# Kernel optimization log

Measured on AMD Instinct MI355X. Metric: run time of the kernel, lower is better.

The kernel has to match this reference:

```python
import jax, jax.numpy as jnp
import numpy as np

N = 8192          # num_people
H = 128           # hidden_dim
ZE = 64           # zone_embed_dim
TE = 32           # temporal_embed_dim
NZ = 100          # num_zones
GRU_IN = H + ZE + TE


def _lin(k, out_d, in_d):
    kw, kb = jax.random.split(k)
    bound = 1.0 / np.sqrt(in_d)
    W = jax.random.uniform(kw, (out_d, in_d), minval=-bound, maxval=bound, dtype=jnp.float32)
    b = jax.random.uniform(kb, (out_d,), minval=-bound, maxval=bound, dtype=jnp.float32)
    return W, b


def setup_inputs() -> dict:
    key = jax.random.key(0)
    ks = jax.random.split(key, 12)
    t = jax.random.uniform(ks[0], (1,), dtype=jnp.float32)
    person_h = jax.random.normal(ks[1], (N, H), dtype=jnp.float32)
    gnn_zone_embeds = jax.random.normal(ks[2], (NZ, ZE), dtype=jnp.float32)
    W_time, b_time = _lin(ks[3], TE, 1)
    W_loc, b_loc = _lin(ks[4], NZ, H)
    Wq, bq = _lin(ks[5], H, H)
    Wk, bk = _lin(ks[6], H, H)
    Wv, bv = _lin(ks[7], H, H)
    W_merge, b_merge = _lin(ks[8], H, 2 * H)
    W_ih, b_ih = _lin(ks[9], 3 * H, GRU_IN)
    W_hh, b_hh = _lin(ks[10], 3 * H, H)
    ln_gamma = jnp.ones((H,), jnp.float32)
    ln_beta = jnp.zeros((H,), jnp.float32)
    return dict(t=t, person_h=person_h, gnn_zone_embeds=gnn_zone_embeds,
                W_time=W_time, b_time=b_time, W_loc=W_loc, b_loc=b_loc,
                Wq=Wq, bq=bq, Wk=Wk, bk=bk, Wv=Wv, bv=bv,
                W_merge=W_merge, b_merge=b_merge,
                W_ih=W_ih, b_ih=b_ih, W_hh=W_hh, b_hh=b_hh,
                ln_gamma=ln_gamma, ln_beta=ln_beta)


def reference(t, person_h, gnn_zone_embeds, W_time, b_time, W_loc, b_loc,
              Wq, bq, Wk, bk, Wv, bv, W_merge, b_merge,
              W_ih, b_ih, W_hh, b_hh, ln_gamma, ln_beta):
    n = person_h.shape[0]
    # spatial context: soft location distribution over zones
    loc_probs = jax.nn.softmax(person_h @ W_loc.T + b_loc, axis=-1)   # [N, NZ]
    spatial_context = loc_probs @ gnn_zone_embeds                     # [N, ZE]
    # leave-one-out social attention == full attention with diagonal masked
    q = person_h @ Wq.T + bq                                          # [N, H]
    k = person_h @ Wk.T + bk
    v = person_h @ Wv.T + bv
    scores = (q @ k.T) / np.sqrt(H).astype(np.float32)                # [N, N]
    diag = jnp.eye(n, dtype=bool)
    scores = jnp.where(diag, -jnp.inf, scores)
    attn = jax.nn.softmax(scores, axis=-1)
    social_context = attn @ v                                         # [N, H]
    h_interacted = jnp.concatenate([person_h, social_context], axis=-1) @ W_merge.T + b_merge
    time_context = jnp.broadcast_to(t.reshape(1, 1), (n, 1)) @ W_time.T + b_time  # [N, TE]
    gru_input = jnp.concatenate([h_interacted, spatial_context, time_context], axis=-1)
    # torch.nn.GRUCell: gates order (reset, update, new)
    gx = gru_input @ W_ih.T + b_ih                                    # [N, 3H]
    gh = person_h @ W_hh.T + b_hh
    xr, xz, xn = jnp.split(gx, 3, axis=-1)
    hr, hz, hn = jnp.split(gh, 3, axis=-1)
    r = jax.nn.sigmoid(xr + hr)
    z = jax.nn.sigmoid(xz + hz)
    ng = jnp.tanh(xn + r * hn)
    h_new = (1.0 - z) * ng + z * person_h
    d = h_new - person_h
    mu = jnp.mean(d, axis=-1, keepdims=True)
    var = jnp.var(d, axis=-1, keepdims=True)
    d = (d - mu) * jax.lax.rsqrt(var + 1e-5) * ln_gamma + ln_beta
    return d
```

## Files before the change

### kernel.cpp

```cpp
#include <hip/hip_runtime.h>


typedef __attribute__((ext_vector_type(8)))  short bf16x8;
typedef __attribute__((ext_vector_type(4)))  float f32x4;
typedef __attribute__((ext_vector_type(16))) float f32x16;
typedef __attribute__((ext_vector_type(4)))  unsigned uint4v;

#define N_P   8192
#define H_D   128
#define NCHNK 8
#define CHLEN (N_P / NCHNK)
#define KVB   64
#define NTIL  (CHLEN / KVB)
#define LDE   384

#if __has_builtin(__builtin_amdgcn_exp2f)
#define EXP2(x) __builtin_amdgcn_exp2f(x)
#else
#define EXP2(x) exp2f(x)
#endif

__device__ __forceinline__ short f2bf(float f) {
  unsigned u = __float_as_uint(f);
  u = (u + 0x7fffu + ((u >> 16) & 1u)) >> 16;
  return (short)u;
}
__device__ __forceinline__ float bf2f(short s) {
  return __uint_as_float(((unsigned)(unsigned short)s) << 16);
}

__device__ __forceinline__ int swzb(int row, int slot, int nslots) {
  return (row * nslots + (slot ^ (row & ((nslots - 1) & 7)))) << 4;
}

__device__ __forceinline__ unsigned cvtpk(float a, float b) {
  unsigned d;
  asm("v_cvt_pk_bf16_f32 %0, %1, %2" : "=v"(d) : "v"(a), "v"(b));
  return d;
}

__device__ __forceinline__ void swap32(unsigned& a, unsigned& b) {
#if __has_builtin(__builtin_amdgcn_permlane32_swap)
  auto r = __builtin_amdgcn_permlane32_swap(a, b, false, false);
  a = r[0]; b = r[1];
#else
  asm volatile("v_permlane32_swap_b32 %0, %1" : "+v"(a), "+v"(b));
#endif
}

typedef __attribute__((address_space(1))) const void GV;
typedef __attribute__((address_space(3))) void LV;
__device__ __forceinline__ void gld_lds16(const void* g, void* l) {
  __builtin_amdgcn_global_load_lds((GV*)g, (LV*)l, 16, 0, 0);
}

__constant__ const float QSCALE = 0.12751551485988857f;
#define LOG2E 1.4426950408889634f

__global__ __launch_bounds__(256) void init_kernel(
    const float* t, const float* W_time, const float* b_time,
    const float* W_loc, const float* b_loc,
    const float* Wq, const float* bq, const float* Wk, const float* bk,
    const float* Wv, const float* bv,
    const float* W_merge, const float* b_merge,
    const float* W_ih, const float* b_ih,
    const float* W_hh, const float* b_hh,
    const float* ph,
    short* W1, float* bias1, short* W_all, float* bias_gx, short* PH2e) {
  const int b = blockIdx.x, tidl = threadIdx.x;
  if (b < 64) {
    int tid = b * 256 + tidl, stride = 64 * 256;
    for (int i = tid; i < 896 * 128; i += stride) {
      int r = i >> 7, k = i & 127;
      float v;
      if (r < 128)      v = Wq[r * 128 + k];
      else if (r < 256) v = Wk[(r - 128) * 128 + k];
      else if (r < 384) v = Wv[(r - 256) * 128 + k];
      else if (r < 484) v = W_loc[(r - 384) * 128 + k];
      else if (r < 868) v = W_hh[(r - 484) * 128 + k];
      else              v = 0.f;
      W1[i] = f2bf(v);
    }
    for (int i = tid; i < 896; i += stride) {
      float v;
      if (i < 128)      v = bq[i];
      else if (i < 256) v = bk[i - 128];
      else if (i < 384) v = bv[i - 256];
      else if (i < 484) v = b_loc[i - 384];
      else if (i < 868) v = b_hh[i - 484];
      else              v = 0.f;
      bias1[i] = v;
    }
  } else if (b < 448) {
    __shared__ float rowj[128];
    const int n = b - 64;
    if (tidl < 128) rowj[tidl] = W_ih[n * 224 + tidl];
    __syncthreads();
    {
      float acc = 0.f;
#pragma unroll 8
      for (int j = 0; j < 128; ++j) acc += rowj[j] * W_merge[j * 256 + tidl];
      W_all[n * 384 + tidl] = f2bf(acc);
    }
    if (tidl < 128) {
      int k2 = 256 + tidl;
      float v;
      if (k2 < 320)      v = W_ih[n * 224 + 128 + (k2 - 256)];
      else if (k2 < 352) v = W_ih[n * 224 + 192 + (k2 - 320)];
      else               v = 0.f;
      W_all[n * 384 + k2] = f2bf(v);
    }
    if (tidl < 64) {
      float p = rowj[tidl] * b_merge[tidl] + rowj[tidl + 64] * b_merge[tidl + 64];
#pragma unroll
      for (int mk = 1; mk < 64; mk <<= 1) p += __shfl_xor(p, mk);
      if (tidl == 0) bias_gx[n] = b_ih[n] + p;
    }
  } else {
    int tid = (b - 448) * 256 + tidl, stride = 1024 * 256;
    for (int i = tid; i < N_P * H_D; i += stride) {
      int r = i >> 7, d = i & 127;
      PH2e[r * LDE + d] = f2bf(ph[i]);
    }
    const float t0 = t[0];
    for (int i = tid; i < N_P * 64; i += stride) {
      int r = i >> 6, j = i & 63;
      float v = (j < 32) ? (t0 * W_time[j] + b_time[j]) : 0.f;
      PH2e[r * LDE + 320 + j] = f2bf(v);
    }
  }
}

template <int MODE, int K>
__global__ __launch_bounds__(256, 3) void gemm64_kernel(
    const short* __restrict__ X, int ldx, const short* __restrict__ W,
    const float* __restrict__ bias,
    short* out_q, short* out_k, short* out_v, float* out_loc, short* out_gh,
    short* out_gx) {
  __shared__ short Xl[64 * 128];
  __shared__ short Wl[128 * 128];
  const int tid = threadIdx.x;
  const int bm = blockIdx.x * 64, bn = blockIdx.y * 128;
  const int l = tid & 63, wid = tid >> 6;
  const int g = l >> 4, c = l & 15;
  const int wr = wid >> 1, wc = wid & 1;
  f32x4 acc[2][4] = {};
  constexpr int KT = K / 128;
#pragma unroll 1
  for (int kt = 0; kt < KT; ++kt) {
    const int k0 = kt * 128;
#pragma unroll
    for (int pass = 0; pass < 4; ++pass) {
      int s = tid + pass * 256;
      int row = s >> 4, p = s & 15;
      int lsl = p ^ (row & 7);
      gld_lds16(X + (size_t)(bm + row) * ldx + k0 + lsl * 8, (char*)Xl + s * 16);
    }
#pragma unroll
    for (int pass = 0; pass < 8; ++pass) {
      int s = tid + pass * 256;
      int row = s >> 4, p = s & 15;
      int lsl = p ^ (row & 7);
      gld_lds16(W + (size_t)(bn + row) * K + k0 + lsl * 8, (char*)Wl + s * 16);
    }
    __syncthreads();
#pragma unroll
    for (int kc = 0; kc < 4; ++kc) {
      bf16x8 a[2], bfr[4];
#pragma unroll
      for (int mi = 0; mi < 2; ++mi)
        a[mi] = *(const bf16x8*)((const char*)Xl + swzb(wr * 32 + mi * 16 + c, kc * 4 + g, 16));
#pragma unroll
      for (int ni = 0; ni < 4; ++ni)
        bfr[ni] = *(const bf16x8*)((const char*)Wl + swzb(wc * 64 + ni * 16 + c, kc * 4 + g, 16));
#pragma unroll
      for (int mi = 0; mi < 2; ++mi)
#pragma unroll
        for (int ni = 0; ni < 4; ++ni)
          acc[mi][ni] = __builtin_amdgcn_mfma_f32_16x16x32_bf16(a[mi], bfr[ni], acc[mi][ni], 0, 0, 0);
    }
    if (kt + 1 < KT) __syncthreads();
  }
#pragma unroll
  for (int mi = 0; mi < 2; ++mi)
#pragma unroll
    for (int ni = 0; ni < 4; ++ni)
#pragma unroll
      for (int r = 0; r < 4; ++r) {
        int row = bm + wr * 32 + mi * 16 + 4 * g + r;
        int col = bn + wc * 64 + ni * 16 + c;
        float val = acc[mi][ni][r] + bias[col];
        if constexpr (MODE == 0) {
          if (col < 128)      out_q[row * 128 + col] = f2bf(val * QSCALE);
          else if (col < 256) out_k[row * 128 + col - 128] = f2bf(val);
          else if (col < 384) out_v[row * 128 + col - 256] = f2bf(val);
          else if (col < 484) out_loc[row * 112 + col - 384] = val;
          else if (col < 868) out_gh[row * 384 + col - 484] = f2bf(val);
        } else {
          out_gx[row * 384 + col] = f2bf(val);
        }
      }
}

__global__ __launch_bounds__(256) void tv_spatial_kernel(const short* __restrict__ vf,
                                                         short* __restrict__ vT,
                                                         const float* __restrict__ locf,
                                                         const float* __restrict__ E,
                                                         short* __restrict__ PH2e) {
  const int b = blockIdx.x, tid = threadIdx.x;
  if (b < 1024) {
    __shared__ short T[32][40];
    int tx = tid & 31, ty = tid >> 5;
    int bi = b >> 2, bd = b & 3;
#pragma unroll
    for (int k = 0; k < 4; ++k)
      T[ty + 8 * k][tx] = vf[(bi * 32 + ty + 8 * k) * 128 + bd * 32 + tx];
    __syncthreads();
#pragma unroll
    for (int k = 0; k < 4; ++k)
      vT[(size_t)(bd * 32 + ty + 8 * k) * N_P + bi * 32 + tx] = T[tx][ty + 8 * k];
  } else {
    __shared__ float pl[4][104];
    int wid = tid >> 6, l = tid & 63;
    int row = (b - 1024) * 4 + wid;
    float v0 = locf[row * 112 + l];
    float v1 = (l + 64 < 100) ? locf[row * 112 + 64 + l] : -1e30f;
    float m = fmaxf(v0, v1);
#pragma unroll
    for (int mk = 1; mk < 64; mk <<= 1) m = fmaxf(m, __shfl_xor(m, mk));
    float p0 = EXP2((v0 - m) * LOG2E);
    float p1 = (l + 64 < 100) ? EXP2((v1 - m) * LOG2E) : 0.f;
    float s = p0 + p1;
#pragma unroll
    for (int mk = 1; mk < 64; mk <<= 1) s += __shfl_xor(s, mk);
    float inv = 1.f / s;
    pl[wid][l] = p0 * inv;
    if (l + 64 < 100) pl[wid][64 + l] = p1 * inv;
    float acc = 0.f;
#pragma unroll 4
    for (int z = 0; z < 100; ++z) acc += pl[wid][z] * E[z * 64 + l];
    PH2e[row * LDE + 256 + l] = f2bf(acc);
  }
}

__global__ __launch_bounds__(256, 2) void attn_kernel(
    const short* __restrict__ qb, const short* __restrict__ kb,
    const short* __restrict__ vT, short* __restrict__ pacc,
    float* __restrict__ pml) {
  __shared__ short Kl[2][KVB * H_D];
  __shared__ short Vl[2][H_D * KVB];
  const int tid = threadIdx.x;
  const int qbk = blockIdx.x >> 3, ch = blockIdx.x & 7;
  const int chbase = ch * CHLEN;
  const int l = tid & 63, wid = tid >> 6;
  const int c32 = l & 31, hi = l >> 5;
  const int qrow0w = qbk * 128 + wid * 32;

  char* ldsK = (char*)&Kl[0][0];
  char* ldsV = (char*)&Vl[0][0];

  auto stage = [&](int b, int tt) {
    const int off = tt * KVB;
#pragma unroll
    for (int j = 0; j < 4; ++j) {
      const int i = tid + j * 256;
      const int kr = i >> 4, ks = (i & 15) ^ (kr & 15);
      gld_lds16(kb + (size_t)(chbase + off + kr) * 128 + ks * 8,
                ldsK + b * 16384 + i * 16);
      const int vr = i >> 3, vs = (i & 7) ^ (vr & 7);
      gld_lds16(vT + (size_t)vr * N_P + chbase + off + vs * 8,
                ldsV + b * 16384 + i * 16);
    }
  };

  bf16x8 qf[8];
#pragma unroll
  for (int sl = 0; sl < 8; ++sl)
    qf[sl] = *(const bf16x8*)(qb + (size_t)(qrow0w + c32) * 128 + sl * 16 + hi * 8);

  bf16x8 ones;
#pragma unroll
  for (int j = 0; j < 8; ++j) ones[j] = (short)0x3F80;

  const int c15 = c32 & 15;
  const int kbase0 = c32 * 256;
  int koff[8];
#pragma unroll
  for (int sl = 0; sl < 8; ++sl) koff[sl] = ((2 * sl + hi) ^ c15) << 4;
  const int xh = (c32 >> 1) & 3, x0 = c32 & 1;
  const int xb = (hi ^ x0) << 4;
  int voff[4], vbase[4];
#pragma unroll
  for (int s4 = 0; s4 < 4; ++s4) voff[s4] = (s4 ^ xh) << 5;
#pragma unroll
  for (int db = 0; db < 4; ++db) vbase[db] = (db * 32 + c32) * 128 + xb;

  f32x16 acc[4] = {};
  f32x16 accl = {};
  float m = -1e30f;

  stage(0, 0);
  asm volatile("s_waitcnt vmcnt(0)" ::: "memory");
  __builtin_amdgcn_s_barrier();
  int cur = 0;

#pragma unroll 1
  for (int t = 0; t < NTIL; ++t) {
    if (t + 1 < NTIL) stage(cur ^ 1, t + 1);

    const int kv0 = chbase + t * KVB;
    const char* Kb = (const char*)&Kl[cur][0];
    const char* Vb = (const char*)&Vl[cur][0];

    f32x16 s0 = {}, s1 = {};
    __builtin_amdgcn_s_setprio(1);
#pragma unroll
    for (int sl = 0; sl < 8; ++sl) {
      bf16x8 k0 = *(const bf16x8*)(Kb + kbase0 + koff[sl]);
      bf16x8 k1 = *(const bf16x8*)(Kb + kbase0 + 8192 + koff[sl]);
      s0 = __builtin_amdgcn_mfma_f32_32x32x16_bf16(k0, qf[sl], s0, 0, 0, 0);
      s1 = __builtin_amdgcn_mfma_f32_32x32x16_bf16(k1, qf[sl], s1, 0, 0, 0);
    }
    __builtin_amdgcn_s_setprio(0);

    if (qrow0w + 32 > kv0 && qrow0w < kv0 + 64) {
      const int qr = qrow0w + c32;
#pragma unroll
      for (int r = 0; r < 16; ++r) {
        const int rowp = (r & 3) + 8 * (r >> 2) + 4 * hi;
        s0[r] = (kv0 + rowp == qr) ? -1e30f : s0[r];
        s1[r] = (kv0 + 32 + rowp == qr) ? -1e30f : s1[r];
      }
    }

    if (t == 0) {
      f32x16 mx;
#pragma unroll
      for (int r = 0; r < 16; ++r) mx[r] = fmaxf(s0[r], s1[r]);
#pragma unroll
      for (int w2 = 8; w2 >= 1; w2 >>= 1)
#pragma unroll
        for (int r = 0; r < w2; ++r) mx[r] = fmaxf(mx[r], mx[r + w2]);
      m = fmaxf(mx[0], __shfl_xor(mx[0], 32));
    }

#pragma unroll
    for (int r = 0; r < 16; ++r) s0[r] = EXP2(s0[r] - m);
#pragma unroll
    for (int r = 0; r < 16; ++r) s1[r] = EXP2(s1[r] - m);

    auto pvslice = [&](const f32x16& ss, int base, int sl4) {
      unsigned dA = cvtpk(ss[base + 0], ss[base + 1]);
      unsigned dB = cvtpk(ss[base + 2], ss[base + 3]);
      unsigned dC = cvtpk(ss[base + 4], ss[base + 5]);
      unsigned dD = cvtpk(ss[base + 6], ss[base + 7]);
      swap32(dA, dC);
      swap32(dB, dD);
      uint4v w = {dA, dB, dC, dD};
      bf16x8 pa = __builtin_bit_cast(bf16x8, w);
#pragma unroll
      for (int db = 0; db < 4; ++db) {
        bf16x8 vfr = *(const bf16x8*)(Vb + vbase[db] + voff[sl4]);
        acc[db] = __builtin_amdgcn_mfma_f32_32x32x16_bf16(pa, vfr, acc[db], 0, 0, 0);
      }
      accl = __builtin_amdgcn_mfma_f32_32x32x16_bf16(pa, ones, accl, 0, 0, 0);
    };
    __builtin_amdgcn_s_setprio(1);
    pvslice(s0, 0, 0);
    pvslice(s0, 8, 1);
    pvslice(s1, 0, 2);
    pvslice(s1, 8, 3);
    __builtin_amdgcn_s_setprio(0);

    if (t + 1 < NTIL) {
      asm volatile("s_waitcnt vmcnt(0)" ::: "memory");
      __builtin_amdgcn_s_barrier();
      asm volatile("" ::: "memory");
    }
    cur ^= 1;
  }

#pragma unroll
  for (int db = 0; db < 4; ++db)
#pragma unroll
    for (int r = 0; r < 16; ++r) {
      const int qr = qrow0w + (r & 3) + 8 * (r >> 2) + 4 * hi;
      pacc[((size_t)ch * N_P + qr) * 128 + db * 32 + c32] = f2bf(acc[db][r]);
    }
  {
    const int rr = (c32 & 3) | (((c32 >> 3) & 3) << 2);
    float own = (((c32 >> 2) & 1) == hi) ? accl[rr] : 0.f;
    float lv = own + __shfl_xor(own, 32);
    if (hi == 0) {
      const int qr = qrow0w + c32;
      pml[((size_t)ch * N_P + qr) * 2]     = m;
      pml[((size_t)ch * N_P + qr) * 2 + 1] = lv;
    }
  }
}

__global__ __launch_bounds__(256) void combine_kernel(const short* __restrict__ pacc,
                                                      const float* __restrict__ pml,
                                                      short* __restrict__ PH2e) {
  int tid = threadIdx.x;
  int row = blockIdx.x * 2 + (tid >> 7);
  int d = tid & 127;
  float mv[NCHNK], lv[NCHNK], M = -1e30f;
#pragma unroll
  for (int cc = 0; cc < NCHNK; ++cc) {
    mv[cc] = pml[(cc * N_P + row) * 2];
    lv[cc] = pml[(cc * N_P + row) * 2 + 1];
    M = fmaxf(M, mv[cc]);
  }
  float L = 0.f, O = 0.f;
#pragma unroll
  for (int cc = 0; cc < NCHNK; ++cc) {
    float w = EXP2(mv[cc] - M);
    L += lv[cc] * w;
    O += bf2f(pacc[((size_t)cc * N_P + row) * 128 + d]) * w;
  }
  PH2e[row * LDE + 128 + d] = f2bf(O / L);
}

__global__ __launch_bounds__(256) void final_kernel(const short* __restrict__ gx,
                                                    const short* __restrict__ gh,
                                                    const float* __restrict__ ph,
                                                    const float* __restrict__ gamma,
                                                    const float* __restrict__ beta,
                                                    float* __restrict__ out) {
  int tid = threadIdx.x, wid = tid >> 6, l = tid & 63;
  int row = blockIdx.x * 4 + wid;
  float dd[2];
#pragma unroll
  for (int half = 0; half < 2; ++half) {
    int d = l + 64 * half;
    float h = ph[row * 128 + d];
    float xr = bf2f(gx[row * 384 + d]),       hr = bf2f(gh[row * 384 + d]);
    float xz = bf2f(gx[row * 384 + 128 + d]), hz = bf2f(gh[row * 384 + 128 + d]);
    float xn = bf2f(gx[row * 384 + 256 + d]), hn = bf2f(gh[row * 384 + 256 + d]);
    float r = 1.f / (1.f + EXP2(-LOG2E * (xr + hr)));
    float z = 1.f / (1.f + EXP2(-LOG2E * (xz + hz)));
    float a = xn + r * hn;
    float ng = 1.f - 2.f / (1.f + EXP2(2.f * LOG2E * a));
    dd[half] = (1.f - z) * (ng - h);
  }
  float s = dd[0] + dd[1], ss = dd[0] * dd[0] + dd[1] * dd[1];
#pragma unroll
  for (int mk = 1; mk < 64; mk <<= 1) {
    s += __shfl_xor(s, mk);
    ss += __shfl_xor(ss, mk);
  }
  float mu = s * (1.f / 128.f);
  float var = ss * (1.f / 128.f) - mu * mu;
  float rs = rsqrtf(var + 1e-5f);
#pragma unroll
  for (int half = 0; half < 2; ++half) {
    int d = l + 64 * half;
    out[row * 128 + d] = (dd[half] - mu) * rs * gamma[d] + beta[d];
  }
}

extern "C" void kernel_launch(void* const* d_in, const int* in_sizes, int n_in,
                              void* d_out, int out_size, void* d_ws, size_t ws_size,
                              hipStream_t stream) {
  const float* t       = (const float*)d_in[0];
  const float* ph      = (const float*)d_in[1];
  const float* E       = (const float*)d_in[2];
  const float* W_time  = (const float*)d_in[3];
  const float* b_time  = (const float*)d_in[4];
  const float* W_loc   = (const float*)d_in[5];
  const float* b_loc   = (const float*)d_in[6];
  const float* Wq      = (const float*)d_in[7];
  const float* bq      = (const float*)d_in[8];
  const float* Wk      = (const float*)d_in[9];
  const float* bk      = (const float*)d_in[10];
  const float* Wv      = (const float*)d_in[11];
  const float* bv      = (const float*)d_in[12];
  const float* W_merge = (const float*)d_in[13];
  const float* b_merge = (const float*)d_in[14];
  const float* W_ih    = (const float*)d_in[15];
  const float* b_ih    = (const float*)d_in[16];
  const float* W_hh    = (const float*)d_in[17];
  const float* b_hh    = (const float*)d_in[18];
  const float* gamma   = (const float*)d_in[19];
  const float* beta    = (const float*)d_in[20];
  float* out = (float*)d_out;

  char* w = (char*)d_ws;
  auto alloc = [&](size_t bytes) {
    char* p = w;
    w += (bytes + 255) & ~(size_t)255;
    return p;
  };
  short* W1     = (short*)alloc(896 * 128 * 2);
  float* bias1  = (float*)alloc(896 * 4);
  short* W_all  = (short*)alloc(384 * 384 * 2);
  float* bias_gx= (float*)alloc(384 * 4);
  short* PH2e   = (short*)alloc((size_t)N_P * LDE * 2);
  short* qbuf   = (short*)alloc((size_t)N_P * 128 * 2);
  short* kbuf   = (short*)alloc((size_t)N_P * 128 * 2);
  short* vf     = (short*)alloc((size_t)N_P * 128 * 2);
  short* vT     = (short*)alloc((size_t)128 * N_P * 2);
  float* locf   = (float*)alloc((size_t)N_P * 112 * 4);
  short* ghf    = (short*)alloc((size_t)N_P * 384 * 2);
  short* gx     = (short*)alloc((size_t)N_P * 384 * 2);
  short* pacc   = (short*)alloc((size_t)NCHNK * N_P * 128 * 2);
  float* pml    = (float*)alloc((size_t)NCHNK * N_P * 2 * 4);

  init_kernel<<<1472, 256, 0, stream>>>(t, W_time, b_time, W_loc, b_loc, Wq, bq,
                                        Wk, bk, Wv, bv, W_merge, b_merge,
                                        W_ih, b_ih, W_hh, b_hh, ph,
                                        W1, bias1, W_all, bias_gx, PH2e);
  gemm64_kernel<0, 128><<<dim3(128, 7), 256, 0, stream>>>(
      PH2e, LDE, W1, bias1, qbuf, kbuf, vf, locf, ghf, nullptr);
  tv_spatial_kernel<<<3072, 256, 0, stream>>>(vf, vT, locf, E, PH2e);
  attn_kernel<<<512, 256, 0, stream>>>(qbuf, kbuf, vT, pacc, pml);
  combine_kernel<<<4096, 256, 0, stream>>>(pacc, pml, PH2e);
  gemm64_kernel<2, 384><<<dim3(128, 3), 256, 0, stream>>>(
      PH2e, LDE, W_all, bias_gx, nullptr, nullptr, nullptr, nullptr, nullptr, gx);
  final_kernel<<<2048, 256, 0, stream>>>(gx, ghf, ph, gamma, beta, out);
}
```

Before: 97.32 us.

## Software-pipeline QK of next tile with softmax/PV and sum row totals on VALU

Restructures the attention loop so the QK^T MFMAs for the next KV tile run alongside the exp2 and PV work of the current tile. K and V staging are split, so K is prefetched two tiles ahead and V is issued after the barrier. The row-sum MFMA against a ones vector is replaced by a scalar fp32 accumulation of the exponentials. The aim is to hide softmax latency behind matrix work and to drop one MFMA per slice. The cost is higher register pressure from holding two score tiles at once, plus more intricate buffer reuse and synchronisation.

```diff
diff --git a/kernel.cpp b/kernel.cpp
--- a/kernel.cpp
+++ b/kernel.cpp
@@ -259,7 +259,7 @@
   char* ldsK = (char*)&Kl[0][0];
   char* ldsV = (char*)&Vl[0][0];
 
-  auto stage = [&](int b, int tt) {
+  auto stageK = [&](int b, int tt) {
     const int off = tt * KVB;
 #pragma unroll
     for (int j = 0; j < 4; ++j) {
@@ -267,6 +267,13 @@
       const int kr = i >> 4, ks = (i & 15) ^ (kr & 15);
       gld_lds16(kb + (size_t)(chbase + off + kr) * 128 + ks * 8,
                 ldsK + b * 16384 + i * 16);
+    }
+  };
+  auto stageV = [&](int b, int tt) {
+    const int off = tt * KVB;
+#pragma unroll
+    for (int j = 0; j < 4; ++j) {
+      const int i = tid + j * 256;
       const int vr = i >> 3, vs = (i & 7) ^ (vr & 7);
       gld_lds16(vT + (size_t)vr * N_P + chbase + off + vs * 8,
                 ldsV + b * 16384 + i * 16);
@@ -277,10 +284,6 @@
 #pragma unroll
   for (int sl = 0; sl < 8; ++sl)
     qf[sl] = *(const bf16x8*)(qb + (size_t)(qrow0w + c32) * 128 + sl * 16 + hi * 8);
-
-  bf16x8 ones;
-#pragma unroll
-  for (int j = 0; j < 8; ++j) ones[j] = (short)0x3F80;
 
   const int c15 = c32 & 15;
   const int kbase0 = c32 * 256;
@@ -296,59 +299,71 @@
   for (int db = 0; db < 4; ++db) vbase[db] = (db * 32 + c32) * 128 + xb;
 
   f32x16 acc[4] = {};
-  f32x16 accl = {};
-  float m = -1e30f;
-
-  stage(0, 0);
-  asm volatile("s_waitcnt vmcnt(0)" ::: "memory");
+  float m = -1e30f, lsum = 0.f;
+
+  auto qkTile = [&](const char* Kb, f32x16& o0, f32x16& o1, int sl) {
+    bf16x8 k0 = *(const bf16x8*)(Kb + kbase0 + koff[sl]);
+    bf16x8 k1 = *(const bf16x8*)(Kb + kbase0 + 8192 + koff[sl]);
+    o0 = __builtin_amdgcn_mfma_f32_32x32x16_bf16(k0, qf[sl], o0, 0, 0, 0);
+    o1 = __builtin_amdgcn_mfma_f32_32x32x16_bf16(k1, qf[sl], o1, 0, 0, 0);
+  };
+  auto maskTile = [&](f32x16& o0, f32x16& o1, int kv0) {
+    if (qrow0w + 32 > kv0 && qrow0w < kv0 + 64) {
+      const int qr = qrow0w + c32;
+#pragma unroll
+      for (int r = 0; r < 16; ++r) {
+        const int rowp = (r & 3) + 8 * (r >> 2) + 4 * hi;
+        o0[r] = (kv0 + rowp == qr) ? -1e30f : o0[r];
+        o1[r] = (kv0 + 32 + rowp == qr) ? -1e30f : o1[r];
+      }
+    }
+  };
+
+  stageK(0, 0); stageV(0, 0); stageK(1, 1); stageV(1, 1);
+  asm volatile("s_waitcnt vmcnt(4)" ::: "memory");
   __builtin_amdgcn_s_barrier();
-  int cur = 0;
+
+  f32x16 s0 = {}, s1 = {};
+#pragma unroll
+  for (int sl = 0; sl < 8; ++sl) qkTile(ldsK, s0, s1, sl);
+  maskTile(s0, s1, chbase);
+  {
+    f32x16 mx;
+#pragma unroll
+    for (int r = 0; r < 16; ++r) mx[r] = fmaxf(s0[r], s1[r]);
+#pragma unroll
+    for (int w2 = 8; w2 >= 1; w2 >>= 1)
+#pragma unroll
+      for (int r = 0; r < w2; ++r) mx[r] = fmaxf(mx[r], mx[r + w2]);
+    m = fmaxf(mx[0], __shfl_xor(mx[0], 32));
+  }
+  __builtin_amdgcn_s_barrier();
 
 #pragma unroll 1
   for (int t = 0; t < NTIL; ++t) {
-    if (t + 1 < NTIL) stage(cur ^ 1, t + 1);
-
-    const int kv0 = chbase + t * KVB;
-    const char* Kb = (const char*)&Kl[cur][0];
-    const char* Vb = (const char*)&Vl[cur][0];
-
-    f32x16 s0 = {}, s1 = {};
+    const int cur = t & 1, nxt = cur ^ 1;
+    if (t + 2 < NTIL) stageK(cur, t + 2);
+
     __builtin_amdgcn_s_setprio(1);
-#pragma unroll
-    for (int sl = 0; sl < 8; ++sl) {
-      bf16x8 k0 = *(const bf16x8*)(Kb + kbase0 + koff[sl]);
-      bf16x8 k1 = *(const bf16x8*)(Kb + kbase0 + 8192 + koff[sl]);
-      s0 = __builtin_amdgcn_mfma_f32_32x32x16_bf16(k0, qf[sl], s0, 0, 0, 0);
-      s1 = __builtin_amdgcn_mfma_f32_32x32x16_bf16(k1, qf[sl], s1, 0, 0, 0);
-    }
-    __builtin_amdgcn_s_setprio(0);
-
-    if (qrow0w + 32 > kv0 && qrow0w < kv0 + 64) {
-      const int qr = qrow0w + c32;
-#pragma unroll
-      for (int r = 0; r < 16; ++r) {
-        const int rowp = (r & 3) + 8 * (r >> 2) + 4 * hi;
-        s0[r] = (kv0 + rowp == qr) ? -1e30f : s0[r];
-        s1[r] = (kv0 + 32 + rowp == qr) ? -1e30f : s1[r];
+    f32x16 sn0 = {}, sn1 = {};
+    if (t + 1 < NTIL) {
+      const char* Kb = ldsK + nxt * 16384;
+#pragma unroll
+      for (int sl = 0; sl < 8; ++sl) {
+        qkTile(Kb, sn0, sn1, sl);
+        s0[2 * sl]     = EXP2(s0[2 * sl] - m);
+        s0[2 * sl + 1] = EXP2(s0[2 * sl + 1] - m);
+        s1[2 * sl]     = EXP2(s1[2 * sl] - m);
+        s1[2 * sl + 1] = EXP2(s1[2 * sl + 1] - m);
       }
-    }
-
-    if (t == 0) {
-      f32x16 mx;
-#pragma unroll
-      for (int r = 0; r < 16; ++r) mx[r] = fmaxf(s0[r], s1[r]);
-#pragma unroll
-      for (int w2 = 8; w2 >= 1; w2 >>= 1)
-#pragma unroll
-        for (int r = 0; r < w2; ++r) mx[r] = fmaxf(mx[r], mx[r + w2]);
-      m = fmaxf(mx[0], __shfl_xor(mx[0], 32));
-    }
-
-#pragma unroll
-    for (int r = 0; r < 16; ++r) s0[r] = EXP2(s0[r] - m);
-#pragma unroll
-    for (int r = 0; r < 16; ++r) s1[r] = EXP2(s1[r] - m);
-
+    } else {
+#pragma unroll
+      for (int r = 0; r < 16; ++r) s0[r] = EXP2(s0[r] - m);
+#pragma unroll
+      for (int r = 0; r < 16; ++r) s1[r] = EXP2(s1[r] - m);
+    }
+
+    const char* Vb = ldsV + cur * 16384;
     auto pvslice = [&](const f32x16& ss, int base, int sl4) {
       unsigned dA = cvtpk(ss[base + 0], ss[base + 1]);
       unsigned dB = cvtpk(ss[base + 2], ss[base + 3]);
@@ -363,9 +378,9 @@
         bf16x8 vfr = *(const bf16x8*)(Vb + vbase[db] + voff[sl4]);
         acc[db] = __builtin_amdgcn_mfma_f32_32x32x16_bf16(pa, vfr, acc[db], 0, 0, 0);
       }
-      accl = __builtin_amdgcn_mfma_f32_32x32x16_bf16(pa, ones, accl, 0, 0, 0);
+#pragma unroll
+      for (int j = 0; j < 8; ++j) lsum += ss[base + j];
     };
-    __builtin_amdgcn_s_setprio(1);
     pvslice(s0, 0, 0);
     pvslice(s0, 8, 1);
     pvslice(s1, 0, 2);
@@ -373,11 +388,12 @@
     __builtin_amdgcn_s_setprio(0);
 
     if (t + 1 < NTIL) {
+      maskTile(sn0, sn1, chbase + (t + 1) * KVB);
+      s0 = sn0; s1 = sn1;
       asm volatile("s_waitcnt vmcnt(0)" ::: "memory");
       __builtin_amdgcn_s_barrier();
-      asm volatile("" ::: "memory");
-    }
-    cur ^= 1;
+      if (t + 2 < NTIL) stageV(cur, t + 2);
+    }
   }
 
 #pragma unroll
@@ -388,9 +404,7 @@
       pacc[((size_t)ch * N_P + qr) * 128 + db * 32 + c32] = f2bf(acc[db][r]);
     }
   {
-    const int rr = (c32 & 3) | (((c32 >> 3) & 3) << 2);
-    float own = (((c32 >> 2) & 1) == hi) ? accl[rr] : 0.f;
-    float lv = own + __shfl_xor(own, 32);
+    float lv = lsum + __shfl_xor(lsum, 32);
     if (hi == 0) {
       const int qr = qrow0w + c32;
       pml[((size_t)ch * N_P + qr) * 2]     = m;
```

After: 101.6 us. +4.4%, slower.

## Fold W_hh gate GEMM into the final GRU input GEMM

Applied to the files above, without the earlier changes.

The hidden-to-hidden GRU projection moves out of the first projection GEMM and into the second GEMM as extra output columns. The weight matrix gains W_hh rows so the r and z gates are pre-summed, and a separate hn block (columns 384-511) is kept for the reset-gated term. This shrinks the first GEMM from 7 to 4 column tiles and removes the separate gh buffer write and read in the final kernel. In exchange the second GEMM grows from 3 to 4 column tiles over K=384, with zero-padded input columns for the hn block.

```diff
diff --git a/kernel.cpp b/kernel.cpp
--- a/kernel.cpp
+++ b/kernel.cpp
@@ -66,58 +66,69 @@
     const float* W_ih, const float* b_ih,
     const float* W_hh, const float* b_hh,
     const float* ph,
-    short* W1, float* bias1, short* W_all, float* bias_gx, short* PH2e) {
+    short* W1, float* bias1, short* W_big, float* bias_big, short* PH2e) {
   const int b = blockIdx.x, tidl = threadIdx.x;
   if (b < 64) {
     int tid = b * 256 + tidl, stride = 64 * 256;
-    for (int i = tid; i < 896 * 128; i += stride) {
+    for (int i = tid; i < 512 * 128; i += stride) {
       int r = i >> 7, k = i & 127;
       float v;
       if (r < 128)      v = Wq[r * 128 + k];
       else if (r < 256) v = Wk[(r - 128) * 128 + k];
       else if (r < 384) v = Wv[(r - 256) * 128 + k];
       else if (r < 484) v = W_loc[(r - 384) * 128 + k];
-      else if (r < 868) v = W_hh[(r - 484) * 128 + k];
       else              v = 0.f;
       W1[i] = f2bf(v);
     }
-    for (int i = tid; i < 896; i += stride) {
+    for (int i = tid; i < 512; i += stride) {
       float v;
       if (i < 128)      v = bq[i];
       else if (i < 256) v = bk[i - 128];
       else if (i < 384) v = bv[i - 256];
       else if (i < 484) v = b_loc[i - 384];
-      else if (i < 868) v = b_hh[i - 484];
       else              v = 0.f;
       bias1[i] = v;
     }
-  } else if (b < 448) {
+  } else if (b < 576) {
     __shared__ float rowj[128];
     const int n = b - 64;
-    if (tidl < 128) rowj[tidl] = W_ih[n * 224 + tidl];
+    if (tidl < 128) rowj[tidl] = (n < 384) ? W_ih[n * 224 + tidl] : 0.f;
     __syncthreads();
     {
       float acc = 0.f;
+      if (n < 384) {
 #pragma unroll 8
-      for (int j = 0; j < 128; ++j) acc += rowj[j] * W_merge[j * 256 + tidl];
-      W_all[n * 384 + tidl] = f2bf(acc);
+        for (int j = 0; j < 128; ++j) acc += rowj[j] * W_merge[j * 256 + tidl];
+      }
+      if (tidl < 128) {
+        if (n < 256)      acc += W_hh[n * 128 + tidl];
+        else if (n >= 384) acc = W_hh[(n - 128) * 128 + tidl];
+      }
+      W_big[n * 384 + tidl] = f2bf(acc);
     }
     if (tidl < 128) {
       int k2 = 256 + tidl;
-      float v;
-      if (k2 < 320)      v = W_ih[n * 224 + 128 + (k2 - 256)];
-      else if (k2 < 352) v = W_ih[n * 224 + 192 + (k2 - 320)];
-      else               v = 0.f;
-      W_all[n * 384 + k2] = f2bf(v);
+      float v = 0.f;
+      if (n < 384) {
+        if (k2 < 320)      v = W_ih[n * 224 + 128 + (k2 - 256)];
+        else if (k2 < 352) v = W_ih[n * 224 + 192 + (k2 - 320)];
+      }
+      W_big[n * 384 + k2] = f2bf(v);
     }
     if (tidl < 64) {
       float p = rowj[tidl] * b_merge[tidl] + rowj[tidl + 64] * b_merge[tidl + 64];
 #pragma unroll
       for (int mk = 1; mk < 64; mk <<= 1) p += __shfl_xor(p, mk);
-      if (tidl == 0) bias_gx[n] = b_ih[n] + p;
+      if (tidl == 0) {
+        float bb;
+        if (n < 256)      bb = b_ih[n] + p + b_hh[n];
+        else if (n < 384) bb = b_ih[n] + p;
+        else              bb = b_hh[n - 128];
+        bias_big[n] = bb;
+      }
     }
   } else {
-    int tid = (b - 448) * 256 + tidl, stride = 1024 * 256;
+    int tid = (b - 576) * 256 + tidl, stride = 1024 * 256;
     for (int i = tid; i < N_P * H_D; i += stride) {
       int r = i >> 7, d = i & 127;
       PH2e[r * LDE + d] = f2bf(ph[i]);
@@ -135,7 +146,7 @@
 __global__ __launch_bounds__(256, 3) void gemm64_kernel(
     const short* __restrict__ X, int ldx, const short* __restrict__ W,
     const float* __restrict__ bias,
-    short* out_q, short* out_k, short* out_v, float* out_loc, short* out_gh,
+    short* out_q, short* out_k, short* out_v, float* out_loc,
     short* out_gx) {
   __shared__ short Xl[64 * 128];
   __shared__ short Wl[128 * 128];
@@ -195,9 +206,8 @@
           else if (col < 256) out_k[row * 128 + col - 128] = f2bf(val);
           else if (col < 384) out_v[row * 128 + col - 256] = f2bf(val);
           else if (col < 484) out_loc[row * 112 + col - 384] = val;
-          else if (col < 868) out_gh[row * 384 + col - 484] = f2bf(val);
         } else {
-          out_gx[row * 384 + col] = f2bf(val);
+          out_gx[row * 512 + col] = f2bf(val);
         }
       }
 }
@@ -422,8 +432,7 @@
   PH2e[row * LDE + 128 + d] = f2bf(O / L);
 }
 
-__global__ __launch_bounds__(256) void final_kernel(const short* __restrict__ gx,
-                                                    const short* __restrict__ gh,
+__global__ __launch_bounds__(256) void final_kernel(const short* __restrict__ gxs,
                                                     const float* __restrict__ ph,
                                                     const float* __restrict__ gamma,
                                                     const float* __restrict__ beta,
@@ -434,12 +443,13 @@
 #pragma unroll
   for (int half = 0; half < 2; ++half) {
     int d = l + 64 * half;
-    float h = ph[row * 128 + d];
-    float xr = bf2f(gx[row * 384 + d]),       hr = bf2f(gh[row * 384 + d]);
-    float xz = bf2f(gx[row * 384 + 128 + d]), hz = bf2f(gh[row * 384 + 128 + d]);
-    float xn = bf2f(gx[row * 384 + 256 + d]), hn = bf2f(gh[row * 384 + 256 + d]);
-    float r = 1.f / (1.f + EXP2(-LOG2E * (xr + hr)));
-    float z = 1.f / (1.f + EXP2(-LOG2E * (xz + hz)));
+    float h  = ph[row * 128 + d];
+    float sr = bf2f(gxs[row * 512 + d]);
+    float sz = bf2f(gxs[row * 512 + 128 + d]);
+    float xn = bf2f(gxs[row * 512 + 256 + d]);
+    float hn = bf2f(gxs[row * 512 + 384 + d]);
+    float r = 1.f / (1.f + EXP2(-LOG2E * sr));
+    float z = 1.f / (1.f + EXP2(-LOG2E * sz));
     float a = xn + r * hn;
     float ng = 1.f - 2.f / (1.f + EXP2(2.f * LOG2E * a));
     dd[half] = (1.f - z) * (ng - h);
@@ -492,31 +502,30 @@
     w += (bytes + 255) & ~(size_t)255;
     return p;
   };
-  short* W1     = (short*)alloc(896 * 128 * 2);
-  float* bias1  = (float*)alloc(896 * 4);
-  short* W_all  = (short*)alloc(384 * 384 * 2);
-  float* bias_gx= (float*)alloc(384 * 4);
-  short* PH2e   = (short*)alloc((size_t)N_P * LDE * 2);
-  short* qbuf   = (short*)alloc((size_t)N_P * 128 * 2);
-  short* kbuf   = (short*)alloc((size_t)N_P * 128 * 2);
-  short* vf     = (short*)alloc((size_t)N_P * 128 * 2);
-  short* vT     = (short*)alloc((size_t)128 * N_P * 2);
-  float* locf   = (float*)alloc((size_t)N_P * 112 * 4);
-  short* ghf    = (short*)alloc((size_t)N_P * 384 * 2);
-  short* gx     = (short*)alloc((size_t)N_P * 384 * 2);
-  short* pacc   = (short*)alloc((size_t)NCHNK * N_P * 128 * 2);
-  float* pml    = (float*)alloc((size_t)NCHNK * N_P * 2 * 4);
-
-  init_kernel<<<1472, 256, 0, stream>>>(t, W_time, b_time, W_loc, b_loc, Wq, bq,
+  short* W1      = (short*)alloc(512 * 128 * 2);
+  float* bias1   = (float*)alloc(512 * 4);
+  short* W_big   = (short*)alloc(512 * 384 * 2);
+  float* bias_big= (float*)alloc(512 * 4);
+  short* PH2e    = (short*)alloc((size_t)N_P * LDE * 2);
+  short* qbuf    = (short*)alloc((size_t)N_P * 128 * 2);
+  short* kbuf    = (short*)alloc((size_t)N_P * 128 * 2);
+  short* vf      = (short*)alloc((size_t)N_P * 128 * 2);
+  short* vT      = (short*)alloc((size_t)128 * N_P * 2);
+  float* locf    = (float*)alloc((size_t)N_P * 112 * 4);
+  short* gxs     = (short*)alloc((size_t)N_P * 512 * 2);
+  short* pacc    = (short*)alloc((size_t)NCHNK * N_P * 128 * 2);
+  float* pml     = (float*)alloc((size_t)NCHNK * N_P * 2 * 4);
+
+  init_kernel<<<1600, 256, 0, stream>>>(t, W_time, b_time, W_loc, b_loc, Wq, bq,
                                         Wk, bk, Wv, bv, W_merge, b_merge,
                                         W_ih, b_ih, W_hh, b_hh, ph,
-                                        W1, bias1, W_all, bias_gx, PH2e);
-  gemm64_kernel<0, 128><<<dim3(128, 7), 256, 0, stream>>>(
-      PH2e, LDE, W1, bias1, qbuf, kbuf, vf, locf, ghf, nullptr);
+                                        W1, bias1, W_big, bias_big, PH2e);
+  gemm64_kernel<0, 128><<<dim3(128, 4), 256, 0, stream>>>(
+      PH2e, LDE, W1, bias1, qbuf, kbuf, vf, locf, nullptr);
   tv_spatial_kernel<<<3072, 256, 0, stream>>>(vf, vT, locf, E, PH2e);
   attn_kernel<<<512, 256, 0, stream>>>(qbuf, kbuf, vT, pacc, pml);
   combine_kernel<<<4096, 256, 0, stream>>>(pacc, pml, PH2e);
-  gemm64_kernel<2, 384><<<dim3(128, 3), 256, 0, stream>>>(
-      PH2e, LDE, W_all, bias_gx, nullptr, nullptr, nullptr, nullptr, nullptr, gx);
-  final_kernel<<<2048, 256, 0, stream>>>(gx, ghf, ph, gamma, beta, out);
-}
+  gemm64_kernel<2, 384><<<dim3(128, 4), 256, 0, stream>>>(
+      PH2e, LDE, W_big, bias_big, nullptr, nullptr, nullptr, nullptr, gxs);
+  final_kernel<<<2048, 256, 0, stream>>>(gxs, ph, gamma, beta, out);
+}
```

Result: faster. 92.36 us (-5.1%).
